# Performance work log

Measured on AMD Instinct MI355X. Metric: run time of the kernel, lower is better.

Reference implementation:

```python
import jax, jax.numpy as jnp
import numpy as np

W = 0.3  # recursive filter weight (thre in original code)


def setup_inputs() -> dict:
    key = jax.random.key(0)
    # [B, C, N, H, W]; recurrence runs along axis 2 (N frames)
    x = jax.random.normal(key, (4, 3, 32, 256, 256), dtype=jnp.float32)
    return {"x": x}


def reference(x):
    # y[0] = x[0]; y[i] = W * x[i] + (1 - W) * y[i-1]  along axis 2
    xs = jnp.moveaxis(x, 2, 0)  # [N, B, C, H, W] so scan runs over leading axis
    y0 = xs[0]

    def step(carry, xi):
        y = W * xi + (1.0 - W) * carry
        return y, y

    _, ys = jax.lax.scan(step, y0, xs[1:])
    out = jnp.concatenate([y0[None], ys], axis=0)  # [N, B, C, H, W]
    return jnp.moveaxis(out, 0, 2)  # back to [B, C, N, H, W]
```

## Files before the change

### kernel.cpp

```cpp
#include <hip/hip_runtime.h>


typedef float vf4 __attribute__((ext_vector_type(4)));

constexpr int   NFR = 32;
constexpr int   HW4 = (256 * 256) / 4;
constexpr int   FPS = 8;
constexpr int   CPB = 64;
constexpr float WF  = 0.3f;
constexpr float OMW = 0.7f;

constexpr float P1  = 0.7f;
constexpr float P2  = P1 * 0.7f;
constexpr float P3  = P2 * 0.7f;
constexpr float P4  = P3 * 0.7f;
constexpr float P5  = P4 * 0.7f;
constexpr float P6  = P5 * 0.7f;
constexpr float P7  = P6 * 0.7f;
constexpr float P8  = P7 * 0.7f;
constexpr float P16 = P8 * P8;

__global__ __launch_bounds__(256, 8) void recfilt_kernel(const vf4* __restrict__ x,
                                                         vf4* __restrict__ y) {
    const int tid = threadIdx.x;
    const int c   = tid & (CPB - 1);
    const int seg = tid >> 6;
    const int q   = blockIdx.x * CPB + c;
    const int bc  = q >> 14;
    const int hw  = q & (HW4 - 1);
    const int base = bc * (NFR * HW4) + seg * (FPS * HW4) + hw;

    vf4 v0 = x[base + 0 * HW4];
    vf4 v1 = x[base + 1 * HW4];
    vf4 v2 = x[base + 2 * HW4];
    vf4 v3 = x[base + 3 * HW4];
    vf4 v4 = x[base + 4 * HW4];
    vf4 v5 = x[base + 5 * HW4];
    vf4 v6 = x[base + 6 * HW4];
    vf4 v7 = x[base + 7 * HW4];

    if (seg != 0) v0 *= WF;
    v1 = WF * v1 + OMW * v0;
    v2 = WF * v2 + OMW * v1;
    v3 = WF * v3 + OMW * v2;
    v4 = WF * v4 + OMW * v3;
    v5 = WF * v5 + OMW * v4;
    v6 = WF * v6 + OMW * v5;
    v7 = WF * v7 + OMW * v6;

    __shared__ vf4 lend[3][CPB];
    if (seg < 3) lend[seg][c] = v7;
    __syncthreads();

    vf4 carry = (vf4)(0.0f);
    if (seg == 1) {
        carry = lend[0][c];
    } else if (seg == 2) {
        carry = lend[1][c] + P8 * lend[0][c];
    } else if (seg == 3) {
        carry = (lend[2][c] + P8 * lend[1][c]) + P16 * lend[0][c];
    }

    vf4 o0 = v0 + P1 * carry;  __builtin_nontemporal_store(o0, &y[base + 0 * HW4]);
    vf4 o1 = v1 + P2 * carry;  __builtin_nontemporal_store(o1, &y[base + 1 * HW4]);
    vf4 o2 = v2 + P3 * carry;  __builtin_nontemporal_store(o2, &y[base + 2 * HW4]);
    vf4 o3 = v3 + P4 * carry;  __builtin_nontemporal_store(o3, &y[base + 3 * HW4]);
    vf4 o4 = v4 + P5 * carry;  __builtin_nontemporal_store(o4, &y[base + 4 * HW4]);
    vf4 o5 = v5 + P6 * carry;  __builtin_nontemporal_store(o5, &y[base + 5 * HW4]);
    vf4 o6 = v6 + P7 * carry;  __builtin_nontemporal_store(o6, &y[base + 6 * HW4]);
    vf4 o7 = v7 + P8 * carry;  __builtin_nontemporal_store(o7, &y[base + 7 * HW4]);
}

extern "C" void kernel_launch(void* const* d_in, const int* in_sizes, int n_in,
                              void* d_out, int out_size, void* d_ws, size_t ws_size,
                              hipStream_t stream) {
    const vf4* x = (const vf4*)d_in[0];
    vf4*       y = (vf4*)d_out;
    const int chains = 12 * HW4;
    const int grid   = chains / CPB;
    recfilt_kernel<<<grid, 256, 0, stream>>>(x, y);
}
```

Baseline: 175.1 us.

## Use wave-local shuffles and software-pipeline three chain batches per wave

```diff
diff --git a/kernel.cpp b/kernel.cpp
--- a/kernel.cpp
+++ b/kernel.cpp
@@ -6,7 +6,6 @@
 constexpr int   NFR = 32;
 constexpr int   HW4 = (256 * 256) / 4;
 constexpr int   FPS = 8;
-constexpr int   CPB = 64;
 constexpr float WF  = 0.3f;
 constexpr float OMW = 0.7f;
 
@@ -20,55 +19,83 @@
 constexpr float P8  = P7 * 0.7f;
 constexpr float P16 = P8 * P8;
 
-__global__ __launch_bounds__(256, 8) void recfilt_kernel(const vf4* __restrict__ x,
+constexpr int DELTA = 4 * NFR * HW4;
+
+static __device__ __forceinline__ vf4 shfl4(vf4 v, int src) {
+    vf4 r;
+    r.x = __shfl(v.x, src);
+    r.y = __shfl(v.y, src);
+    r.z = __shfl(v.z, src);
+    r.w = __shfl(v.w, src);
+    return r;
+}
+
+#define LOADS(p, B)              \
+    p##0 = x[(B) + 0 * HW4];     \
+    p##1 = x[(B) + 1 * HW4];     \
+    p##2 = x[(B) + 2 * HW4];     \
+    p##3 = x[(B) + 3 * HW4];     \
+    p##4 = x[(B) + 4 * HW4];     \
+    p##5 = x[(B) + 5 * HW4];     \
+    p##6 = x[(B) + 6 * HW4];     \
+    p##7 = x[(B) + 7 * HW4];
+
+#define PREFIX(p)                       \
+    p##0 = s0 ? p##0 : WF * p##0;       \
+    p##1 = WF * p##1 + OMW * p##0;      \
+    p##2 = WF * p##2 + OMW * p##1;      \
+    p##3 = WF * p##3 + OMW * p##2;      \
+    p##4 = WF * p##4 + OMW * p##3;      \
+    p##5 = WF * p##5 + OMW * p##4;      \
+    p##6 = WF * p##6 + OMW * p##5;      \
+    p##7 = WF * p##7 + OMW * p##6;
+
+#define CLOSE(p, B)                                                        \
+    {                                                                      \
+        const vf4 e0 = shfl4(p##7, c);                                     \
+        const vf4 e1 = shfl4(p##7, c + 16);                                \
+        const vf4 e2 = shfl4(p##7, c + 32);                                \
+        vf4 carry = (vf4)(0.0f);                                           \
+        if (seg == 1)      carry = e0;                                     \
+        else if (seg == 2) carry = e1 + P8 * e0;                           \
+        else if (seg == 3) carry = (e2 + P8 * e1) + P16 * e0;              \
+        vf4 o;                                                             \
+        o = p##0 + P1 * carry; __builtin_nontemporal_store(o, &y[(B) + 0 * HW4]); \
+        o = p##1 + P2 * carry; __builtin_nontemporal_store(o, &y[(B) + 1 * HW4]); \
+        o = p##2 + P3 * carry; __builtin_nontemporal_store(o, &y[(B) + 2 * HW4]); \
+        o = p##3 + P4 * carry; __builtin_nontemporal_store(o, &y[(B) + 3 * HW4]); \
+        o = p##4 + P5 * carry; __builtin_nontemporal_store(o, &y[(B) + 4 * HW4]); \
+        o = p##5 + P6 * carry; __builtin_nontemporal_store(o, &y[(B) + 5 * HW4]); \
+        o = p##6 + P7 * carry; __builtin_nontemporal_store(o, &y[(B) + 6 * HW4]); \
+        o = p##7 + P8 * carry; __builtin_nontemporal_store(o, &y[(B) + 7 * HW4]); \
+    }
+
+__global__ __launch_bounds__(256, 4) void recfilt_kernel(const vf4* __restrict__ x,
                                                          vf4* __restrict__ y) {
-    const int tid = threadIdx.x;
-    const int c   = tid & (CPB - 1);
-    const int seg = tid >> 6;
-    const int q   = blockIdx.x * CPB + c;
-    const int bc  = q >> 14;
-    const int hw  = q & (HW4 - 1);
+    const int tid  = threadIdx.x;
+    const int wv   = (blockIdx.x << 2) + (tid >> 6);
+    const int lane = tid & 63;
+    const int c    = lane & 15;
+    const int seg  = lane >> 4;
+    const bool s0  = (seg == 0);
+
+    const int q    = (wv << 4) + c;
+    const int bc   = q >> 14;
+    const int hw   = q & (HW4 - 1);
     const int base = bc * (NFR * HW4) + seg * (FPS * HW4) + hw;
 
-    vf4 v0 = x[base + 0 * HW4];
-    vf4 v1 = x[base + 1 * HW4];
-    vf4 v2 = x[base + 2 * HW4];
-    vf4 v3 = x[base + 3 * HW4];
-    vf4 v4 = x[base + 4 * HW4];
-    vf4 v5 = x[base + 5 * HW4];
-    vf4 v6 = x[base + 6 * HW4];
-    vf4 v7 = x[base + 7 * HW4];
+    vf4 a0, a1, a2, a3, a4, a5, a6, a7;
+    vf4 b0, b1, b2, b3, b4, b5, b6, b7;
 
-    if (seg != 0) v0 *= WF;
-    v1 = WF * v1 + OMW * v0;
-    v2 = WF * v2 + OMW * v1;
-    v3 = WF * v3 + OMW * v2;
-    v4 = WF * v4 + OMW * v3;
-    v5 = WF * v5 + OMW * v4;
-    v6 = WF * v6 + OMW * v5;
-    v7 = WF * v7 + OMW * v6;
-
-    __shared__ vf4 lend[3][CPB];
-    if (seg < 3) lend[seg][c] = v7;
-    __syncthreads();
-
-    vf4 carry = (vf4)(0.0f);
-    if (seg == 1) {
-        carry = lend[0][c];
-    } else if (seg == 2) {
-        carry = lend[1][c] + P8 * lend[0][c];
-    } else if (seg == 3) {
-        carry = (lend[2][c] + P8 * lend[1][c]) + P16 * lend[0][c];
-    }
-
-    vf4 o0 = v0 + P1 * carry;  __builtin_nontemporal_store(o0, &y[base + 0 * HW4]);
-    vf4 o1 = v1 + P2 * carry;  __builtin_nontemporal_store(o1, &y[base + 1 * HW4]);
-    vf4 o2 = v2 + P3 * carry;  __builtin_nontemporal_store(o2, &y[base + 2 * HW4]);
-    vf4 o3 = v3 + P4 * carry;  __builtin_nontemporal_store(o3, &y[base + 3 * HW4]);
-    vf4 o4 = v4 + P5 * carry;  __builtin_nontemporal_store(o4, &y[base + 4 * HW4]);
-    vf4 o5 = v5 + P6 * carry;  __builtin_nontemporal_store(o5, &y[base + 5 * HW4]);
-    vf4 o6 = v6 + P7 * carry;  __builtin_nontemporal_store(o6, &y[base + 6 * HW4]);
-    vf4 o7 = v7 + P8 * carry;  __builtin_nontemporal_store(o7, &y[base + 7 * HW4]);
+    LOADS(a, base)
+    PREFIX(a)
+    LOADS(b, base + DELTA)
+    CLOSE(a, base)
+    PREFIX(b)
+    LOADS(a, base + 2 * DELTA)
+    CLOSE(b, base + DELTA)
+    PREFIX(a)
+    CLOSE(a, base + 2 * DELTA)
 }
 
 extern "C" void kernel_launch(void* const* d_in, const int* in_sizes, int n_in,
@@ -76,7 +103,5 @@
                               hipStream_t stream) {
     const vf4* x = (const vf4*)d_in[0];
     vf4*       y = (vf4*)d_out;
-    const int chains = 12 * HW4;
-    const int grid   = chains / CPB;
-    recfilt_kernel<<<grid, 256, 0, stream>>>(x, y);
+    recfilt_kernel<<<1024, 256, 0, stream>>>(x, y);
 }
```

Result: no change. 175.8 us (+0.4%).
